# Optimization experiments

Hardware: AMD Instinct MI355X
Metric: run time of the kernel (lower is better)

## Reference

```python
import jax, jax.numpy as jnp
import numpy as np

B, S, N = 8, 2048, 1024

def setup_inputs() -> dict:
    key = jax.random.key(0)
    k1, k2, k3 = jax.random.split(key, 3)
    outer = jax.random.normal(k1, (B, S, N), dtype=jnp.float32)
    extended_attention_mask = jnp.zeros((B, 1, S), dtype=jnp.float32)
    # torch Linear init scale ~ 1/sqrt(n)
    sc = 1.0 / np.sqrt(N)
    Wk = jax.random.normal(k2, (N, N), dtype=jnp.float32) * sc
    bk = jnp.zeros((N,), dtype=jnp.float32)
    Wq = jax.random.normal(k3, (N, N), dtype=jnp.float32) * sc
    bq = jnp.zeros((N,), dtype=jnp.float32)
    return {"outer": outer, "extended_attention_mask": extended_attention_mask,
            "Wk": Wk, "bk": bk, "Wq": Wq, "bq": bq}

def reference(outer, extended_attention_mask, Wk, bk, Wq, bq):
    # k = sigmoid(outer @ Wk^T + bk), q = sigmoid(outer @ Wq^T + bq)
    k = jax.nn.sigmoid(jnp.einsum('bsn,mn->bsm', outer, Wk) + bk)  # [B,S,N]
    q = jax.nn.sigmoid(jnp.einsum('bsn,mn->bsm', outer, Wq) + bq)  # [B,S,N]
    # scores: q @ k^T + mask -> [B,S,S]
    s = jnp.einsum('bqn,bkn->bqk', q, k) + extended_attention_mask
    attn = jax.nn.softmax(s, axis=-1)
    out = jnp.einsum('bqk,bkn->bqn', attn, outer)  # [B,S,N]
    return out.sum(-1)  # [B,S]
```

## Files before the change

### kernel.cpp

```cpp
#include <hip/hip_runtime.h>
#include <hip/hip_bf16.h>

#define BB 8
#define SS 2048
#define NN 1024
#define MT (BB*SS)
#define NKC 16
#define NPC 32

typedef __attribute__((ext_vector_type(8))) short bf16x8;
typedef __attribute__((ext_vector_type(4))) float f32x4;
typedef unsigned short u16;
typedef unsigned int u32;

__device__ __forceinline__ u16 f2bf(float f) {
  u32 u = __float_as_uint(f);
  u += 0x7fff + ((u >> 16) & 1);
  return (u16)(u >> 16);
}
__device__ __forceinline__ float bf2f(u16 h) {
  return __uint_as_float(((u32)h) << 16);
}

typedef __attribute__((address_space(1))) void GV;
typedef __attribute__((address_space(3))) void LV;
__device__ __forceinline__ void cp16(const void* g, void* l) {
  __builtin_amdgcn_global_load_lds((GV*)g, (LV*)l, 16, 0, 0);
}

__global__ __launch_bounds__(256) void prep_x_kernel(const float* __restrict__ outer,
                                                     const float* __restrict__ mask,
                                                     u16* __restrict__ Xb,
                                                     float* __restrict__ r,
                                                     float* __restrict__ kb) {
  int w = threadIdx.x >> 6, lane = threadIdx.x & 63;
  int row = blockIdx.x * 4 + w;
  const float4* src = (const float4*)(outer + (size_t)row * NN);
  ushort4* dst = (ushort4*)(Xb + (size_t)row * NN);
  float s = 0.f;
#pragma unroll
  for (int u = 0; u < 4; u++) {
    int idx = lane + u * 64;
    float4 v = src[idx];
    ushort4 o;
    o.x = f2bf(v.x); o.y = f2bf(v.y); o.z = f2bf(v.z); o.w = f2bf(v.w);
    dst[idx] = o;
    s += (v.x + v.y) + (v.z + v.w);
  }
#pragma unroll
  for (int off = 1; off < 64; off <<= 1) s += __shfl_xor(s, off);
  if (lane == 0) { r[row] = s; kb[row] = mask[row]; }
}

__global__ __launch_bounds__(256) void prep_w_kernel(const float* __restrict__ Wq,
                                                     const float* __restrict__ Wk,
                                                     const float* __restrict__ bq,
                                                     const float* __restrict__ bk,
                                                     u16* __restrict__ Wb,
                                                     float* __restrict__ bb) {
  int idx = blockIdx.x * 256 + threadIdx.x;
  int e = idx * 4;
  int rowm = e >> 10;
  int col = e & 1023;
  const float* srcp = (rowm < NN) ? (Wq + (size_t)rowm * NN + col)
                                  : (Wk + (size_t)(rowm - NN) * NN + col);
  float4 v = *(const float4*)srcp;
  ushort4 o; o.x = f2bf(v.x); o.y = f2bf(v.y); o.z = f2bf(v.z); o.w = f2bf(v.w);
  *(ushort4*)(Wb + (size_t)e) = o;
  if (idx < 2 * NN) bb[idx] = (idx < NN) ? bq[idx] : bk[idx - NN];
}

__global__ __launch_bounds__(256, 3) void gemm1_kernel(const u16* __restrict__ X,
                                                       const u16* __restrict__ W,
                                                       const float* __restrict__ bb,
                                                       u16* __restrict__ C,
                                                       float* __restrict__ kb) {
  __shared__ u16 lA[2][128 * 32];
  __shared__ u16 lB[2][128 * 32];
  int bid = blockIdx.x;
  int tn = ((bid & 7) << 1) | ((bid >> 3) & 1);
  int tm = bid >> 4;
  int tid = threadIdx.x;
  int w = tid >> 6, lane = tid & 63;
  int wr = w >> 1, wc = w & 1;
  int srow = tid >> 2;
  int scol = (tid & 3) * 8;
  const u16* gA = X + (size_t)(tm * 128 + srow) * NN + scol;
  const u16* gB = W + (size_t)(tn * 128 + srow) * NN + scol;
  u16* dA0 = &lA[0][srow * 32 + scol];
  u16* dA1 = &lA[1][srow * 32 + scol];
  u16* dB0 = &lB[0][srow * 32 + scol];
  u16* dB1 = &lB[1][srow * 32 + scol];
  int quad = lane >> 4;
  const u16* pa0 = &lA[0][(wr * 64 + (lane & 15)) * 32 + quad * 8];
  const u16* pb0 = &lB[0][(wc * 64 + (lane & 15)) * 32 + quad * 8];
  const u16* pa1 = pa0 + 128 * 32;
  const u16* pb1 = pb0 + 128 * 32;
  f32x4 acc[4][4] = {};
  for (int kk = 0; kk < NN; kk += 64) {
    cp16(gA, dA0);           cp16(gA + 64 * NN, dA0 + 64 * 32);
    cp16(gB, dB0);           cp16(gB + 64 * NN, dB0 + 64 * 32);
    cp16(gA + 32, dA1);      cp16(gA + 32 + 64 * NN, dA1 + 64 * 32);
    cp16(gB + 32, dB1);      cp16(gB + 32 + 64 * NN, dB1 + 64 * 32);
    gA += 64; gB += 64;
    __syncthreads();
    {
      bf16x8 af[4], bf[4];
#pragma unroll
      for (int i = 0; i < 4; i++) af[i] = *(const bf16x8*)(pa0 + i * 16 * 32);
#pragma unroll
      for (int j = 0; j < 4; j++) bf[j] = *(const bf16x8*)(pb0 + j * 16 * 32);
#pragma unroll
      for (int i = 0; i < 4; i++)
#pragma unroll
        for (int j = 0; j < 4; j++)
          acc[i][j] = __builtin_amdgcn_mfma_f32_16x16x32_bf16(af[i], bf[j], acc[i][j], 0, 0, 0);
    }
    {
      bf16x8 af[4], bf[4];
#pragma unroll
      for (int i = 0; i < 4; i++) af[i] = *(const bf16x8*)(pa1 + i * 16 * 32);
#pragma unroll
      for (int j = 0; j < 4; j++) bf[j] = *(const bf16x8*)(pb1 + j * 16 * 32);
#pragma unroll
      for (int i = 0; i < 4; i++)
#pragma unroll
        for (int j = 0; j < 4; j++)
          acc[i][j] = __builtin_amdgcn_mfma_f32_16x16x32_bf16(af[i], bf[j], acc[i][j], 0, 0, 0);
    }
    __syncthreads();
  }
  int quad4 = quad * 4;
  int colb = tn * 128 + wc * 64 + (lane & 15);
  bool khalf = (tn >= 8);
#pragma unroll
  for (int i = 0; i < 4; i++) {
    float rsum[4] = {0.f, 0.f, 0.f, 0.f};
#pragma unroll
    for (int j = 0; j < 4; j++) {
      int col = colb + j * 16;
      float bias = bb[col];
#pragma unroll
      for (int rg = 0; rg < 4; rg++) {
        int row = tm * 128 + wr * 64 + i * 16 + quad4 + rg;
        float v = acc[i][j][rg] + bias;
        float sg = 1.0f / (1.0f + __expf(-v));
        u16 h = f2bf(sg - 0.5f);
        C[(size_t)row * 2048 + col] = h;
        rsum[rg] += bf2f(h);
      }
    }
    if (khalf) {
#pragma unroll
      for (int rg = 0; rg < 4; rg++) {
        float s = rsum[rg];
#pragma unroll
        for (int off = 1; off < 16; off <<= 1) s += __shfl_xor(s, off);
        if ((lane & 15) == 0) {
          int row = tm * 128 + wr * 64 + i * 16 + quad4 + rg;
          atomicAdd(&kb[row], 0.5f * s);
        }
      }
    }
  }
}

__global__ __launch_bounds__(256, 3) void flash_kernel(const u16* __restrict__ C,
                                                       const float* __restrict__ kb,
                                                       const float* __restrict__ r,
                                                       float* __restrict__ pm,
                                                       float* __restrict__ pl,
                                                       float* __restrict__ pt) {
  __shared__ u16 lA[2][128 * 32];
  __shared__ u16 lB[2][128 * 32];
  int bid = blockIdx.x;
  int b  = bid & 7;
  int kc = (bid >> 3) & 15;
  int qt = bid >> 7;
  int tid = threadIdx.x;
  int w = tid >> 6, lane = tid & 63;
  int wr = w >> 1, wc = w & 1;
  int srow = tid >> 2;
  int scol = (tid & 3) * 8;
  int key0 = kc * 128;
  const u16* gA = C + (size_t)(b * SS + qt * 128 + srow) * 2048 + scol;
  const u16* gB = C + (size_t)(b * SS + key0 + srow) * 2048 + 1024 + scol;
  u16* dA0 = &lA[0][srow * 32 + scol];
  u16* dA1 = &lA[1][srow * 32 + scol];
  u16* dB0 = &lB[0][srow * 32 + scol];
  u16* dB1 = &lB[1][srow * 32 + scol];
  int quad = lane >> 4;
  const u16* pa0 = &lA[0][(wr * 64 + (lane & 15)) * 32 + quad * 8];
  const u16* pb0 = &lB[0][(wc * 64 + (lane & 15)) * 32 + quad * 8];
  const u16* pa1 = pa0 + 128 * 32;
  const u16* pb1 = pb0 + 128 * 32;

  f32x4 acc[4][4] = {};
  for (int kk = 0; kk < NN; kk += 64) {
    cp16(gA, dA0);           cp16(gA + 64 * 2048, dA0 + 64 * 32);
    cp16(gB, dB0);           cp16(gB + 64 * 2048, dB0 + 64 * 32);
    cp16(gA + 32, dA1);      cp16(gA + 32 + 64 * 2048, dA1 + 64 * 32);
    cp16(gB + 32, dB1);      cp16(gB + 32 + 64 * 2048, dB1 + 64 * 32);
    gA += 64; gB += 64;
    __syncthreads();
    {
      bf16x8 af[4], bf[4];
#pragma unroll
      for (int i = 0; i < 4; i++) af[i] = *(const bf16x8*)(pa0 + i * 16 * 32);
#pragma unroll
      for (int j = 0; j < 4; j++) bf[j] = *(const bf16x8*)(pb0 + j * 16 * 32);
#pragma unroll
      for (int i = 0; i < 4; i++)
#pragma unroll
        for (int j = 0; j < 4; j++)
          acc[i][j] = __builtin_amdgcn_mfma_f32_16x16x32_bf16(af[i], bf[j], acc[i][j], 0, 0, 0);
    }
    {
      bf16x8 af[4], bf[4];
#pragma unroll
      for (int i = 0; i < 4; i++) af[i] = *(const bf16x8*)(pa1 + i * 16 * 32);
#pragma unroll
      for (int j = 0; j < 4; j++) bf[j] = *(const bf16x8*)(pb1 + j * 16 * 32);
#pragma unroll
      for (int i = 0; i < 4; i++)
#pragma unroll
        for (int j = 0; j < 4; j++)
          acc[i][j] = __builtin_amdgcn_mfma_f32_16x16x32_bf16(af[i], bf[j], acc[i][j], 0, 0, 0);
    }
    __syncthreads();
  }

  float kbv[4], rv[4];
  int colg = b * SS + key0 + wc * 64 + (lane & 15);
#pragma unroll
  for (int j = 0; j < 4; j++) { kbv[j] = kb[colg + j * 16]; rv[j] = r[colg + j * 16]; }
  int quad4 = quad * 4;
  int chunk = kc * 2 + wc;
#pragma unroll
  for (int i = 0; i < 4; i++) {
#pragma unroll
    for (int rg = 0; rg < 4; rg++) {
      float lg[4];
      float tmax = -1e30f;
#pragma unroll
      for (int j = 0; j < 4; j++) { lg[j] = acc[i][j][rg] + kbv[j]; tmax = fmaxf(tmax, lg[j]); }
#pragma unroll
      for (int off = 1; off < 16; off <<= 1) tmax = fmaxf(tmax, __shfl_xor(tmax, off));
      float rs = 0.f, rt = 0.f;
#pragma unroll
      for (int j = 0; j < 4; j++) {
        float p = __expf(lg[j] - tmax);
        rs += p; rt += p * rv[j];
      }
#pragma unroll
      for (int off = 1; off < 16; off <<= 1) { rs += __shfl_xor(rs, off); rt += __shfl_xor(rt, off); }
      if ((lane & 15) == 0) {
        int grow = b * SS + qt * 128 + wr * 64 + i * 16 + quad4 + rg;
        pm[grow * NPC + chunk] = tmax;
        pl[grow * NPC + chunk] = rs;
        pt[grow * NPC + chunk] = rt;
      }
    }
  }
}

__global__ __launch_bounds__(256) void fixup_kernel(const float* __restrict__ pm,
                                                    const float* __restrict__ pl,
                                                    const float* __restrict__ pt,
                                                    float* __restrict__ out) {
  int row = blockIdx.x * 256 + threadIdx.x;
  float Mx = -1e30f;
#pragma unroll
  for (int c = 0; c < NPC; c++) Mx = fmaxf(Mx, pm[row * NPC + c]);
  float L = 0.f, T = 0.f;
#pragma unroll
  for (int c = 0; c < NPC; c++) {
    float a = __expf(pm[row * NPC + c] - Mx);
    L += pl[row * NPC + c] * a;
    T += pt[row * NPC + c] * a;
  }
  out[row] = T / L;
}

extern "C" void kernel_launch(void* const* d_in, const int* in_sizes, int n_in,
                              void* d_out, int out_size, void* d_ws, size_t ws_size,
                              hipStream_t stream) {
  const float* outer = (const float*)d_in[0];
  const float* mask  = (const float*)d_in[1];
  const float* Wk    = (const float*)d_in[2];
  const float* bk    = (const float*)d_in[3];
  const float* Wq    = (const float*)d_in[4];
  const float* bq    = (const float*)d_in[5];
  float* out = (float*)d_out;

  char* ws = (char*)d_ws;
  size_t off = 0;
  auto alloc = [&](size_t bytes) -> void* {
    void* p = ws + off;
    off = (off + bytes + 255) & ~(size_t)255;
    return p;
  };
  u16* Xb  = (u16*)alloc((size_t)MT * NN * 2);
  u16* Wb  = (u16*)alloc((size_t)2048 * NN * 2);
  u16* Cq  = (u16*)alloc((size_t)MT * 2048 * 2);
  float* bb = (float*)alloc(2048 * 4);
  float* rr = (float*)alloc((size_t)MT * 4);
  float* kb = (float*)alloc((size_t)MT * 4);
  float* pm = (float*)alloc((size_t)MT * NPC * 4);
  float* pl = (float*)alloc((size_t)MT * NPC * 4);
  float* pt = (float*)alloc((size_t)MT * NPC * 4);

  prep_x_kernel<<<dim3(MT / 4), dim3(256), 0, stream>>>(outer, mask, Xb, rr, kb);
  prep_w_kernel<<<dim3(2048), dim3(256), 0, stream>>>(Wq, Wk, bq, bk, Wb, bb);
  gemm1_kernel<<<dim3(2048), dim3(256), 0, stream>>>(Xb, Wb, bb, Cq, kb);
  flash_kernel<<<dim3(2048), dim3(256), 0, stream>>>(Cq, kb, rr, pm, pl, pt);
  fixup_kernel<<<dim3(MT / 256), dim3(256), 0, stream>>>(pm, pl, pt, out);
}
```

Measured before the change: 289.2 us.

## Use 256x256 tiles with double-buffered async LDS pipeline in both GEMMs

Both GEMM kernels (projection and QK scores) now share a templated core. It uses 256x256 output tiles with 512 threads (8 waves, each 128x64), so each block does more reuse per loaded byte. Global-to-LDS loads are double-buffered, with explicit vmcnt waits and raw barriers, so the next K-slice loads while MFMAs run on the current one, and MFMA bursts are raised in priority with s_setprio. Block-to-tile mapping is also remapped with XCD awareness. The cost is larger LDS use (128KB per block), a larger register footprint from 32 accumulators, and fewer blocks (512), which may hurt occupancy and balance.

After: 299.0 us. +3.4%, slower.

```diff
diff --git a/kernel.cpp b/kernel.cpp
--- a/kernel.cpp
+++ b/kernel.cpp
@@ -5,8 +5,8 @@
 #define SS 2048
 #define NN 1024
 #define MT (BB*SS)
-#define NKC 16
 #define NPC 32
+#define NG 16
 
 typedef __attribute__((ext_vector_type(8))) short bf16x8;
 typedef __attribute__((ext_vector_type(4))) float f32x4;
@@ -27,6 +27,11 @@
 __device__ __forceinline__ void cp16(const void* g, void* l) {
   __builtin_amdgcn_global_load_lds((GV*)g, (LV*)l, 16, 0, 0);
 }
+
+#define WAITV8 asm volatile("s_waitcnt vmcnt(8)" ::: "memory")
+#define WAITV0 asm volatile("s_waitcnt vmcnt(0)" ::: "memory")
+#define BARX   __builtin_amdgcn_s_barrier()
+#define FEN    asm volatile("" ::: "memory")
 
 __global__ __launch_bounds__(256) void prep_x_kernel(const float* __restrict__ outer,
                                                      const float* __restrict__ mask,
@@ -70,79 +75,93 @@
   if (idx < 2 * NN) bb[idx] = (idx < NN) ? bq[idx] : bk[idx - NN];
 }
 
-__global__ __launch_bounds__(256, 3) void gemm1_kernel(const u16* __restrict__ X,
+template<int LDG>
+__device__ __forceinline__ void gemm_core(const u16* gA0, const u16* gB0,
+                                          u16* lA, u16* lB, int tid,
+                                          f32x4 (&acc)[8][4]) {
+  const int row_t = tid >> 2;
+  const int c8 = (tid & 3) << 3;
+  const int lane = tid & 63;
+  const int w = tid >> 6;
+  const int wr = w >> 2, wc = w & 3;
+  const int l15 = lane & 15, quad = lane >> 4;
+  const u16* sA = gA0 + (size_t)row_t * LDG + c8;
+  const u16* sB = gB0 + (size_t)row_t * LDG + c8;
+  u16* dA = lA + row_t * 32 + c8;
+  u16* dB = lB + row_t * 32 + c8;
+  const u16* pa = lA + (wr * 128 + l15) * 32 + quad * 8;
+  const u16* pb = lB + (wc * 64 + l15) * 32 + quad * 8;
+
+  auto STAGE = [&](int s, int kt) {
+    const u16* a_ = sA + kt * 64;
+    const u16* b_ = sB + kt * 64;
+    u16* la_ = dA + s * 16384;
+    u16* lb_ = dB + s * 16384;
+    cp16(a_, la_);                cp16(a_ + 128 * LDG, la_ + 4096);
+    cp16(a_ + 32, la_ + 8192);    cp16(a_ + 32 + 128 * LDG, la_ + 12288);
+    cp16(b_, lb_);                cp16(b_ + 128 * LDG, lb_ + 4096);
+    cp16(b_ + 32, lb_ + 8192);    cp16(b_ + 32 + 128 * LDG, lb_ + 12288);
+  };
+
+  auto COMP = [&](int s) {
+#pragma unroll
+    for (int ks = 0; ks < 2; ++ks) {
+      bf16x8 af[8], bf[4];
+#pragma unroll
+      for (int i = 0; i < 8; ++i) af[i] = *(const bf16x8*)(pa + s * 16384 + ks * 8192 + i * 512);
+#pragma unroll
+      for (int j = 0; j < 4; ++j) bf[j] = *(const bf16x8*)(pb + s * 16384 + ks * 8192 + j * 512);
+      __builtin_amdgcn_s_setprio(1);
+#pragma unroll
+      for (int i = 0; i < 8; ++i)
+#pragma unroll
+        for (int j = 0; j < 4; ++j)
+          acc[i][j] = __builtin_amdgcn_mfma_f32_16x16x32_bf16(af[i], bf[j], acc[i][j], 0, 0, 0);
+      __builtin_amdgcn_s_setprio(0);
+    }
+  };
+
+  STAGE(0, 0);
+#pragma unroll 1
+  for (int k = 0; k < NG - 2; k += 2) {
+    STAGE(1, k + 1); WAITV8; BARX; FEN; COMP(0); BARX;
+    STAGE(0, k + 2); WAITV8; BARX; FEN; COMP(1); BARX;
+  }
+  STAGE(1, NG - 1); WAITV8; BARX; FEN; COMP(0); BARX;
+  WAITV0; BARX; FEN; COMP(1);
+}
+
+__global__ __launch_bounds__(512, 2) void gemm1_kernel(const u16* __restrict__ X,
                                                        const u16* __restrict__ W,
                                                        const float* __restrict__ bb,
                                                        u16* __restrict__ C,
                                                        float* __restrict__ kb) {
-  __shared__ u16 lA[2][128 * 32];
-  __shared__ u16 lB[2][128 * 32];
+  __shared__ u16 lA[2 * 16384];
+  __shared__ u16 lB[2 * 16384];
   int bid = blockIdx.x;
-  int tn = ((bid & 7) << 1) | ((bid >> 3) & 1);
-  int tm = bid >> 4;
+  int xcd = bid & 7, idx = bid >> 3;
+  int tm = xcd * 8 + (idx & 7);
+  int tn = idx >> 3;
   int tid = threadIdx.x;
-  int w = tid >> 6, lane = tid & 63;
-  int wr = w >> 1, wc = w & 1;
-  int srow = tid >> 2;
-  int scol = (tid & 3) * 8;
-  const u16* gA = X + (size_t)(tm * 128 + srow) * NN + scol;
-  const u16* gB = W + (size_t)(tn * 128 + srow) * NN + scol;
-  u16* dA0 = &lA[0][srow * 32 + scol];
-  u16* dA1 = &lA[1][srow * 32 + scol];
-  u16* dB0 = &lB[0][srow * 32 + scol];
-  u16* dB1 = &lB[1][srow * 32 + scol];
-  int quad = lane >> 4;
-  const u16* pa0 = &lA[0][(wr * 64 + (lane & 15)) * 32 + quad * 8];
-  const u16* pb0 = &lB[0][(wc * 64 + (lane & 15)) * 32 + quad * 8];
-  const u16* pa1 = pa0 + 128 * 32;
-  const u16* pb1 = pb0 + 128 * 32;
-  f32x4 acc[4][4] = {};
-  for (int kk = 0; kk < NN; kk += 64) {
-    cp16(gA, dA0);           cp16(gA + 64 * NN, dA0 + 64 * 32);
-    cp16(gB, dB0);           cp16(gB + 64 * NN, dB0 + 64 * 32);
-    cp16(gA + 32, dA1);      cp16(gA + 32 + 64 * NN, dA1 + 64 * 32);
-    cp16(gB + 32, dB1);      cp16(gB + 32 + 64 * NN, dB1 + 64 * 32);
-    gA += 64; gB += 64;
-    __syncthreads();
-    {
-      bf16x8 af[4], bf[4];
-#pragma unroll
-      for (int i = 0; i < 4; i++) af[i] = *(const bf16x8*)(pa0 + i * 16 * 32);
-#pragma unroll
-      for (int j = 0; j < 4; j++) bf[j] = *(const bf16x8*)(pb0 + j * 16 * 32);
-#pragma unroll
-      for (int i = 0; i < 4; i++)
-#pragma unroll
-        for (int j = 0; j < 4; j++)
-          acc[i][j] = __builtin_amdgcn_mfma_f32_16x16x32_bf16(af[i], bf[j], acc[i][j], 0, 0, 0);
-    }
-    {
-      bf16x8 af[4], bf[4];
-#pragma unroll
-      for (int i = 0; i < 4; i++) af[i] = *(const bf16x8*)(pa1 + i * 16 * 32);
-#pragma unroll
-      for (int j = 0; j < 4; j++) bf[j] = *(const bf16x8*)(pb1 + j * 16 * 32);
-#pragma unroll
-      for (int i = 0; i < 4; i++)
-#pragma unroll
-        for (int j = 0; j < 4; j++)
-          acc[i][j] = __builtin_amdgcn_mfma_f32_16x16x32_bf16(af[i], bf[j], acc[i][j], 0, 0, 0);
-    }
-    __syncthreads();
-  }
-  int quad4 = quad * 4;
-  int colb = tn * 128 + wc * 64 + (lane & 15);
-  bool khalf = (tn >= 8);
-#pragma unroll
-  for (int i = 0; i < 4; i++) {
+  f32x4 acc[8][4] = {};
+  gemm_core<1024>(X + (size_t)tm * 256 * 1024, W + (size_t)tn * 256 * 1024,
+                  lA, lB, tid, acc);
+
+  int lane = tid & 63, w = tid >> 6;
+  int wr = w >> 2, wc = w & 3, l15 = lane & 15, quad = lane >> 4;
+  int colb = tn * 256 + wc * 64 + l15;
+  bool khalf = (tn >= 4);
+  int rowb = tm * 256 + wr * 128 + quad * 4;
+#pragma unroll
+  for (int i = 0; i < 8; ++i) {
     float rsum[4] = {0.f, 0.f, 0.f, 0.f};
 #pragma unroll
-    for (int j = 0; j < 4; j++) {
+    for (int j = 0; j < 4; ++j) {
       int col = colb + j * 16;
       float bias = bb[col];
 #pragma unroll
-      for (int rg = 0; rg < 4; rg++) {
-        int row = tm * 128 + wr * 64 + i * 16 + quad4 + rg;
+      for (int rg = 0; rg < 4; ++rg) {
+        int row = rowb + i * 16 + rg;
         float v = acc[i][j][rg] + bias;
         float sg = 1.0f / (1.0f + __expf(-v));
         u16 h = f2bf(sg - 0.5f);
@@ -152,113 +171,66 @@
     }
     if (khalf) {
 #pragma unroll
-      for (int rg = 0; rg < 4; rg++) {
+      for (int rg = 0; rg < 4; ++rg) {
         float s = rsum[rg];
 #pragma unroll
         for (int off = 1; off < 16; off <<= 1) s += __shfl_xor(s, off);
-        if ((lane & 15) == 0) {
-          int row = tm * 128 + wr * 64 + i * 16 + quad4 + rg;
-          atomicAdd(&kb[row], 0.5f * s);
-        }
-      }
-    }
-  }
-}
-
-__global__ __launch_bounds__(256, 3) void flash_kernel(const u16* __restrict__ C,
+        if (l15 == 0) atomicAdd(&kb[rowb + i * 16 + rg], 0.5f * s);
+      }
+    }
+  }
+}
+
+__global__ __launch_bounds__(512, 2) void flash_kernel(const u16* __restrict__ Cq,
                                                        const float* __restrict__ kb,
                                                        const float* __restrict__ r,
                                                        float* __restrict__ pm,
                                                        float* __restrict__ pl,
                                                        float* __restrict__ pt) {
-  __shared__ u16 lA[2][128 * 32];
-  __shared__ u16 lB[2][128 * 32];
+  __shared__ u16 lA[2 * 16384];
+  __shared__ u16 lB[2 * 16384];
   int bid = blockIdx.x;
-  int b  = bid & 7;
-  int kc = (bid >> 3) & 15;
-  int qt = bid >> 7;
+  int b = bid & 7;
+  int idx = bid >> 3;
+  int qt = idx >> 3;
+  int kc = idx & 7;
   int tid = threadIdx.x;
-  int w = tid >> 6, lane = tid & 63;
-  int wr = w >> 1, wc = w & 1;
-  int srow = tid >> 2;
-  int scol = (tid & 3) * 8;
-  int key0 = kc * 128;
-  const u16* gA = C + (size_t)(b * SS + qt * 128 + srow) * 2048 + scol;
-  const u16* gB = C + (size_t)(b * SS + key0 + srow) * 2048 + 1024 + scol;
-  u16* dA0 = &lA[0][srow * 32 + scol];
-  u16* dA1 = &lA[1][srow * 32 + scol];
-  u16* dB0 = &lB[0][srow * 32 + scol];
-  u16* dB1 = &lB[1][srow * 32 + scol];
-  int quad = lane >> 4;
-  const u16* pa0 = &lA[0][(wr * 64 + (lane & 15)) * 32 + quad * 8];
-  const u16* pb0 = &lB[0][(wc * 64 + (lane & 15)) * 32 + quad * 8];
-  const u16* pa1 = pa0 + 128 * 32;
-  const u16* pb1 = pb0 + 128 * 32;
-
-  f32x4 acc[4][4] = {};
-  for (int kk = 0; kk < NN; kk += 64) {
-    cp16(gA, dA0);           cp16(gA + 64 * 2048, dA0 + 64 * 32);
-    cp16(gB, dB0);           cp16(gB + 64 * 2048, dB0 + 64 * 32);
-    cp16(gA + 32, dA1);      cp16(gA + 32 + 64 * 2048, dA1 + 64 * 32);
-    cp16(gB + 32, dB1);      cp16(gB + 32 + 64 * 2048, dB1 + 64 * 32);
-    gA += 64; gB += 64;
-    __syncthreads();
-    {
-      bf16x8 af[4], bf[4];
-#pragma unroll
-      for (int i = 0; i < 4; i++) af[i] = *(const bf16x8*)(pa0 + i * 16 * 32);
-#pragma unroll
-      for (int j = 0; j < 4; j++) bf[j] = *(const bf16x8*)(pb0 + j * 16 * 32);
-#pragma unroll
-      for (int i = 0; i < 4; i++)
-#pragma unroll
-        for (int j = 0; j < 4; j++)
-          acc[i][j] = __builtin_amdgcn_mfma_f32_16x16x32_bf16(af[i], bf[j], acc[i][j], 0, 0, 0);
-    }
-    {
-      bf16x8 af[4], bf[4];
-#pragma unroll
-      for (int i = 0; i < 4; i++) af[i] = *(const bf16x8*)(pa1 + i * 16 * 32);
-#pragma unroll
-      for (int j = 0; j < 4; j++) bf[j] = *(const bf16x8*)(pb1 + j * 16 * 32);
-#pragma unroll
-      for (int i = 0; i < 4; i++)
-#pragma unroll
-        for (int j = 0; j < 4; j++)
-          acc[i][j] = __builtin_amdgcn_mfma_f32_16x16x32_bf16(af[i], bf[j], acc[i][j], 0, 0, 0);
-    }
-    __syncthreads();
-  }
-
+  f32x4 acc[8][4] = {};
+  gemm_core<2048>(Cq + (size_t)(b * SS + qt * 256) * 2048,
+                  Cq + (size_t)(b * SS + kc * 256) * 2048 + 1024,
+                  lA, lB, tid, acc);
+
+  int lane = tid & 63, w = tid >> 6;
+  int wr = w >> 2, wc = w & 3, l15 = lane & 15, quad = lane >> 4;
   float kbv[4], rv[4];
-  int colg = b * SS + key0 + wc * 64 + (lane & 15);
-#pragma unroll
-  for (int j = 0; j < 4; j++) { kbv[j] = kb[colg + j * 16]; rv[j] = r[colg + j * 16]; }
-  int quad4 = quad * 4;
-  int chunk = kc * 2 + wc;
-#pragma unroll
-  for (int i = 0; i < 4; i++) {
-#pragma unroll
-    for (int rg = 0; rg < 4; rg++) {
+  int colg = b * SS + kc * 256 + wc * 64 + l15;
+#pragma unroll
+  for (int j = 0; j < 4; ++j) { kbv[j] = kb[colg + j * 16]; rv[j] = r[colg + j * 16]; }
+  int chunk = kc * 4 + wc;
+  int rowb = b * SS + qt * 256 + wr * 128 + quad * 4;
+#pragma unroll
+  for (int i = 0; i < 8; ++i) {
+#pragma unroll
+    for (int rg = 0; rg < 4; ++rg) {
       float lg[4];
       float tmax = -1e30f;
 #pragma unroll
-      for (int j = 0; j < 4; j++) { lg[j] = acc[i][j][rg] + kbv[j]; tmax = fmaxf(tmax, lg[j]); }
+      for (int j = 0; j < 4; ++j) { lg[j] = acc[i][j][rg] + kbv[j]; tmax = fmaxf(tmax, lg[j]); }
 #pragma unroll
       for (int off = 1; off < 16; off <<= 1) tmax = fmaxf(tmax, __shfl_xor(tmax, off));
       float rs = 0.f, rt = 0.f;
 #pragma unroll
-      for (int j = 0; j < 4; j++) {
+      for (int j = 0; j < 4; ++j) {
         float p = __expf(lg[j] - tmax);
         rs += p; rt += p * rv[j];
       }
 #pragma unroll
       for (int off = 1; off < 16; off <<= 1) { rs += __shfl_xor(rs, off); rt += __shfl_xor(rt, off); }
-      if ((lane & 15) == 0) {
-        int grow = b * SS + qt * 128 + wr * 64 + i * 16 + quad4 + rg;
-        pm[grow * NPC + chunk] = tmax;
-        pl[grow * NPC + chunk] = rs;
-        pt[grow * NPC + chunk] = rt;
+      if (l15 == 0) {
+        int grow = rowb + i * 16 + rg;
+        pm[(size_t)grow * NPC + chunk] = tmax;
+        pl[(size_t)grow * NPC + chunk] = rs;
+        pt[(size_t)grow * NPC + chunk] = rt;
       }
     }
   }
@@ -312,7 +284,7 @@
 
   prep_x_kernel<<<dim3(MT / 4), dim3(256), 0, stream>>>(outer, mask, Xb, rr, kb);
   prep_w_kernel<<<dim3(2048), dim3(256), 0, stream>>>(Wq, Wk, bq, bk, Wb, bb);
-  gemm1_kernel<<<dim3(2048), dim3(256), 0, stream>>>(Xb, Wb, bb, Cq, kb);
-  flash_kernel<<<dim3(2048), dim3(256), 0, stream>>>(Cq, kb, rr, pm, pl, pt);
+  gemm1_kernel<<<dim3(512), dim3(512), 0, stream>>>(Xb, Wb, bb, Cq, kb);
+  flash_kernel<<<dim3(512), dim3(512), 0, stream>>>(Cq, kb, rr, pm, pl, pt);
   fixup_kernel<<<dim3(MT / 256), dim3(256), 0, stream>>>(pm, pl, pt, out);
 }
```
